# Kernel tuning notes

Measured on AMD Instinct MI355X. Metric: run time of the kernel, lower is better.

## Reference

```python
import jax, jax.numpy as jnp
import numpy as np

EPS = 1e-5
ALPHA = 0.05   # propalpha
GDEP = 2       # gcn_depth
LAYERS = 3     # gcn_layers
NUM_TCN = 2    # num_layer tcn units per encoder


def conv1x1(W, b, x):
    # 1x1 Conv2d on [B,C,N,1]: pure channel mix
    return jnp.einsum('oc,bcnl->bonl', W, x) + b[None, :, None, None]


def tcn_unit(Wf, bf, Wg, bg, h):
    # gated TCN unit: tanh(filter) * sigmoid(gate), 1x1 convs (L==1)
    return jnp.tanh(conv1x1(Wf, bf, h)) * jax.nn.sigmoid(conv1x1(Wg, bg, h))


def mixprop(x, A, W, b):
    # MTGNN mixprop: add self-loops, row-normalize, gdep propagation steps,
    # concat hops on channel dim, 1x1 conv mlp. A: [N,N] or [B,N,N].
    N = A.shape[-1]
    A = A + jnp.eye(N, dtype=A.dtype)
    A = A / A.sum(-1, keepdims=True)
    h = x
    outs = [h]
    for _ in range(GDEP):
        if A.ndim == 2:
            hn = jnp.einsum('vw,bcwl->bcvl', A, h)
        else:
            hn = jnp.einsum('bvw,bcwl->bcvl', A, h)
        h = ALPHA * x + (1.0 - ALPHA) * hn
        outs.append(h)
    ho = jnp.concatenate(outs, axis=1)  # [B,(GDEP+1)*C,N,1]
    return conv1x1(W, b, ho)


def layernorm(x, w, b):
    # LayerNorm over (C,N,1) of [B,C,N,1]; idx=arange(N) selects full affine
    mu = x.mean(axis=(1, 2, 3), keepdims=True)
    var = x.var(axis=(1, 2, 3), keepdims=True)
    return (x - mu) / jnp.sqrt(var + EPS) * w[None] + b[None]


def setup_inputs() -> dict:
    key = jax.random.key(0)
    B, N, E, H, S, T = 8, 2048, 32, 128, 256, 12
    ks = jax.random.split(key, 32)
    s = 0.05
    inp = {
        'x': jax.random.normal(ks[0], (B, E, N, 1), jnp.float32),
        'dy_graph': jax.random.uniform(ks[1], (B, N, N), jnp.float32),
        'static_graph': jax.random.uniform(ks[2], (N, N), jnp.float32),
        'spatial_emb': jax.random.normal(ks[3], (B, 32, N, 1), jnp.float32),
        'temporal_d_emb': jax.random.normal(ks[4], (B, 32, N, 1), jnp.float32),
        'temporal_w_emb': jax.random.normal(ks[5], (B, 32, N, 1), jnp.float32),
        'enc_Wf': s * jax.random.normal(ks[6], (LAYERS, NUM_TCN, H, H), jnp.float32),
        'enc_bf': s * jax.random.normal(ks[7], (LAYERS, NUM_TCN, H), jnp.float32),
        'enc_Wg': s * jax.random.normal(ks[8], (LAYERS, NUM_TCN, H, H), jnp.float32),
        'enc_bg': s * jax.random.normal(ks[9], (LAYERS, NUM_TCN, H), jnp.float32),
        'skip_W': s * jax.random.normal(ks[10], (LAYERS, S, H), jnp.float32),
        'skip_b': s * jax.random.normal(ks[11], (LAYERS, S), jnp.float32),
        'norm_w': jnp.ones((LAYERS, E, N, 1), jnp.float32),
        'norm_b': jnp.zeros((LAYERS, E, N, 1), jnp.float32),
        'g0_W': s * jax.random.normal(ks[12], (LAYERS, E, (GDEP + 1) * E), jnp.float32),
        'g0_b': s * jax.random.normal(ks[13], (LAYERS, E), jnp.float32),
        'g1_W': s * jax.random.normal(ks[14], (LAYERS, E, (GDEP + 1) * E), jnp.float32),
        'g1_b': s * jax.random.normal(ks[15], (LAYERS, E), jnp.float32),
        'g2_W': s * jax.random.normal(ks[16], (LAYERS, E, (GDEP + 1) * E), jnp.float32),
        'g2_b': s * jax.random.normal(ks[17], (LAYERS, E), jnp.float32),
        'skipE_W': s * jax.random.normal(ks[18], (S, E), jnp.float32),
        'skipE_b': s * jax.random.normal(ks[19], (S,), jnp.float32),
        'end_W': s * jax.random.normal(ks[20], (T, S), jnp.float32),
        'end_b': s * jax.random.normal(ks[21], (T,), jnp.float32),
    }
    return inp


def reference(x, dy_graph, static_graph, spatial_emb, temporal_d_emb, temporal_w_emb,
              enc_Wf, enc_bf, enc_Wg, enc_bg, skip_W, skip_b, norm_w, norm_b,
              g0_W, g0_b, g1_W, g1_b, g2_W, g2_b, skipE_W, skipE_b, end_W, end_b):
    adp = dy_graph
    skip = 0.0
    for i in range(LAYERS):
        residual = x
        hidden = jnp.concatenate([x, spatial_emb, temporal_d_emb, temporal_w_emb], axis=1)
        for j in range(NUM_TCN):
            hidden = tcn_unit(enc_Wf[i, j], enc_bf[i, j], enc_Wg[i, j], enc_bg[i, j], hidden)
        skip = conv1x1(skip_W[i], skip_b[i], hidden) + skip
        x = (mixprop(x, static_graph, g0_W[i], g0_b[i])
             + mixprop(x, adp, g1_W[i], g1_b[i])
             + mixprop(x, jnp.swapaxes(adp, -1, -2), g2_W[i], g2_b[i]))
        x = x + residual
        x = jax.nn.relu(layernorm(x, norm_w[i], norm_b[i]))
    skip = conv1x1(skipE_W, skipE_b, x) + skip
    return conv1x1(end_W, end_b, skip)  # [B, seq_length, N, 1]
```

## Files before the change

### kernel.cpp

```cpp
#include <hip/hip_runtime.h>
#include <stdint.h>


typedef uint16_t u16;
typedef uint32_t u32;
typedef __attribute__((ext_vector_type(8))) short s8v;
typedef __attribute__((ext_vector_type(4))) float f4v;

#define MFMA16(a,b,c) __builtin_amdgcn_mfma_f32_16x16x32_bf16(a,b,c,0,0,0)

__device__ __forceinline__ float b2f(u16 u){ union{u32 i; float f;} x; x.i=(u32)u<<16; return x.f; }
__device__ __forceinline__ u16 f2b(float f){
  u32 u = __builtin_bit_cast(u32, f);
  u32 r = (u + 0x7fffu + ((u >> 16) & 1u)) >> 16;
  return (u16)r;
}

__device__ __forceinline__ void gld16(const void* g, void* l) {
  __builtin_amdgcn_global_load_lds(
      (const __attribute__((address_space(1))) void*)g,
      (__attribute__((address_space(3))) void*)l, 16, 0, 0);
}

__global__ __launch_bounds__(256) void kdetect(const u16* __restrict__ x, int* __restrict__ flag)
{
  const int i = blockIdx.x*256 + threadIdx.x;
  const uint4 v = ((const uint4*)x)[i];
  const u32 w[4] = {v.x, v.y, v.z, v.w};
  int cnt = 0;
  #pragma unroll
  for (int e = 0; e < 4; e++) {
    if ((w[e] & 0x7F80u) == 0x7F80u) cnt++;
    if (((w[e] >> 16) & 0x7F80u) == 0x7F80u) cnt++;
  }
  const unsigned long long m = __ballot(cnt != 0);
  if (m && (threadIdx.x & 63) == 0) atomicOr(flag, 1);
}

__global__ __launch_bounds__(256) void kcvt4(const void* __restrict__ src, u16* __restrict__ dst,
                                             int n4, const int* __restrict__ flag)
{
  if (!*flag) return;
  const int i = blockIdx.x*256 + threadIdx.x;
  if (i >= n4) return;
  const float4 v = ((const float4*)src)[i];
  u16 o[4]; o[0]=f2b(v.x); o[1]=f2b(v.y); o[2]=f2b(v.z); o[3]=f2b(v.w);
  *(uint2*)(dst + (long)i*4) = *(uint2*)o;
}

struct CvtTab { const void* s[18]; u16* d[18]; int n4[18]; };
__global__ __launch_bounds__(256) void kcvt_small(CvtTab tb, const int* __restrict__ flag)
{
  const int e = blockIdx.y;
  const int i = blockIdx.x*256 + threadIdx.x;
  if (i >= tb.n4[e]) return;
  if (*flag) {
    const float4 v = ((const float4*)tb.s[e])[i];
    u16 o[4]; o[0]=f2b(v.x); o[1]=f2b(v.y); o[2]=f2b(v.z); o[3]=f2b(v.w);
    *(uint2*)(tb.d[e] + (long)i*4) = *(uint2*)o;
  } else {
    *(uint2*)(tb.d[e] + (long)i*4) = ((const uint2*)tb.s[e])[i];
  }
}

__global__ __launch_bounds__(256) void kcvtT(
    const void* __restrict__ src, u16* __restrict__ dyb, u16* __restrict__ dytb,
    float* __restrict__ rsum, float* __restrict__ csum, const int* __restrict__ flag)
{
  __shared__ alignas(16) u32 tt[64][32];
  const int tid = threadIdx.x;
  const int b = blockIdx.z;
  const long r0 = (long)blockIdx.y*64;
  const long c0 = (long)blockIdx.x*64;
  const int rp = tid>>3, c8 = (tid&7)*8;
  const long base = (long)b*4194304;
  const int fl = *flag;

  u16 lo[8], hi[8];
  const long gl = base + (r0 + 2*rp)*2048 + c0 + c8;
  const long gh = gl + 2048;
  if (fl) {
    const float* sl = (const float*)src + gl;
    const float* sh = (const float*)src + gh;
    const float4 a0 = ((const float4*)sl)[0], a1 = ((const float4*)sl)[1];
    const float4 b0 = ((const float4*)sh)[0], b1 = ((const float4*)sh)[1];
    lo[0]=f2b(a0.x); lo[1]=f2b(a0.y); lo[2]=f2b(a0.z); lo[3]=f2b(a0.w);
    lo[4]=f2b(a1.x); lo[5]=f2b(a1.y); lo[6]=f2b(a1.z); lo[7]=f2b(a1.w);
    hi[0]=f2b(b0.x); hi[1]=f2b(b0.y); hi[2]=f2b(b0.z); hi[3]=f2b(b0.w);
    hi[4]=f2b(b1.x); hi[5]=f2b(b1.y); hi[6]=f2b(b1.z); hi[7]=f2b(b1.w);
    *(uint4*)(dyb + gl) = *(uint4*)lo;
    *(uint4*)(dyb + gh) = *(uint4*)hi;
  } else {
    *(uint4*)lo = *((const uint4*)((const u16*)src + gl));
    *(uint4*)hi = *((const uint4*)((const u16*)src + gh));
  }
  float rsl = 0.f, rsh = 0.f;
  #pragma unroll
  for (int e = 0; e < 8; e++) {
    rsl += b2f(lo[e]); rsh += b2f(hi[e]);
    const int c = c8 + e;
    tt[c][rp ^ ((c & 0x38) >> 1)] = (u32)lo[e] | ((u32)hi[e] << 16);
  }
  rsl += __shfl_down(rsl, 4, 8); rsl += __shfl_down(rsl, 2, 8); rsl += __shfl_down(rsl, 1, 8);
  rsh += __shfl_down(rsh, 4, 8); rsh += __shfl_down(rsh, 2, 8); rsh += __shfl_down(rsh, 1, 8);
  if ((tid & 7) == 0) {
    atomicAdd(rsum + b*2048 + r0 + 2*rp,     rsl);
    atomicAdd(rsum + b*2048 + r0 + 2*rp + 1, rsh);
  }
  __syncthreads();

  const int c = tid>>2, j4 = (tid&3)*8;
  const int sw = (c & 0x38) >> 1;
  u32 q[8];
  *(uint4*)&q[0] = *(const uint4*)&tt[c][j4 ^ sw];
  *(uint4*)&q[4] = *(const uint4*)&tt[c][(j4 + 4) ^ sw];
  float cs = 0.f;
  #pragma unroll
  for (int e = 0; e < 8; e++) { cs += b2f((u16)q[e]); cs += b2f((u16)(q[e] >> 16)); }
  cs += __shfl_down(cs, 2, 4); cs += __shfl_down(cs, 1, 4);
  u16* dp = dytb + base + (c0 + c)*2048 + r0 + 2*j4;
  *(uint4*)(dp)     = *(uint4*)&q[0];
  *(uint4*)(dp + 8) = *(uint4*)&q[4];
  if ((tid & 3) == 0) atomicAdd(csum + b*2048 + c0 + c, cs);
}

__global__ void kfin(float* __restrict__ v){
  const int i = blockIdx.x*256 + threadIdx.x;
  v[i] = 1.f/(1.f + v[i]);
}

struct PG {
  const u16* Ac0; const u16* Ac1; const u16* Ac2;
  const u16* Ar0; const u16* Ar1;
  const int* flag;
  long ab0, ab1, ab2;
  const u16* X0; const u16* X1; const u16* X2;
  const float* R0; const float* R1; const float* R2;
  long rb0, rb1, rb2;
  u16* O0; u16* O1; u16* O2;
};

__global__ __launch_bounds__(256) void kprops(PG p, long x_bs, long o_bs)
{
  __shared__ u16 Al[4][64][64];
  __shared__ u16 Xl[4][32][64];
  const int tid = threadIdx.x, wave = tid>>6, lane = tid&63;
  const int lw = lane&15, quad = lane>>4;
  const int wr = wave>>1, wc = wave&1;
  const int v0 = blockIdx.x*64;
  const int b = blockIdx.y, g = blockIdx.z;
  const int fl = *p.flag;
  const u16* Ag; long ab; const u16* Xg; const float* Rg; long rb; u16* Og;
  if (g == 0)      { Ag = fl ? p.Ac0 : p.Ar0; ab = p.ab0; Xg = p.X0; Rg = p.R0; rb = p.rb0; Og = p.O0; }
  else if (g == 1) { Ag = fl ? p.Ac1 : p.Ar1; ab = p.ab1; Xg = p.X1; Rg = p.R1; rb = p.rb1; Og = p.O1; }
  else             { Ag = p.Ac2;              ab = p.ab2; Xg = p.X2; Rg = p.R2; rb = p.rb2; Og = p.O2; }
  const u16* Ab = Ag + (long)b*ab;
  const u16* Xb = Xg + (long)b*x_bs;

  const int srow = wave*8 + (lane>>3);
  const int skc  = lane&7;
  const long soff = (long)((skc ^ (srow&7))*8);
  const u16* srcA0 = Ab + (long)(v0 + srow)*2048 + soff;
  const u16* srcA1 = Ab + (long)(v0 + 32 + srow)*2048 + soff;
  const u16* srcX  = Xb + (long)srow*2048 + soff;

#define STAGE(tt) do { const int bb_=(tt)&3; const long k0_=(long)(tt)*64;          \
    gld16(srcA0 + k0_, (void*)((char*)&Al[bb_][0][0]  + wave*1024));                \
    gld16(srcA1 + k0_, (void*)((char*)&Al[bb_][32][0] + wave*1024));                \
    gld16(srcX  + k0_, (void*)((char*)&Xl[bb_][0][0]  + wave*1024)); } while(0)

  f4v acc0 = {0.f,0.f,0.f,0.f}, acc1 = {0.f,0.f,0.f,0.f};
  const int arow0 = wr*32 + lw;
  const int arow1 = wr*32 + 16 + lw;
  const int xrow  = wc*16 + lw;
  const int sw    = lw & 7;
  const int q0    = (quad ^ sw)*8;
  const int q1    = ((quad ^ sw) ^ 4)*8;

  STAGE(0); STAGE(1); STAGE(2);

  #pragma unroll 1
  for (int t = 0; t < 32; t++) {
    if (t < 30)       asm volatile("s_waitcnt vmcnt(6)" ::: "memory");
    else if (t == 30) asm volatile("s_waitcnt vmcnt(3)" ::: "memory");
    else              asm volatile("s_waitcnt vmcnt(0)" ::: "memory");
    __builtin_amdgcn_s_barrier();
    __builtin_amdgcn_sched_barrier(0);
    const int bb = t&3;
    s8v x0  = *(const s8v*)&Xl[bb][xrow][q0];
    s8v a00 = *(const s8v*)&Al[bb][arow0][q0];
    s8v a10 = *(const s8v*)&Al[bb][arow1][q0];
    s8v x1  = *(const s8v*)&Xl[bb][xrow][q1];
    s8v a01 = *(const s8v*)&Al[bb][arow0][q1];
    s8v a11 = *(const s8v*)&Al[bb][arow1][q1];
    acc0 = MFMA16(a00, x0, acc0);
    acc1 = MFMA16(a10, x0, acc1);
    acc0 = MFMA16(a01, x1, acc0);
    acc1 = MFMA16(a11, x1, acc1);
    if (t <= 28) STAGE(t+3);
  }
#undef STAGE

  const int c = wc*16 + lw;
  const float* rp = Rg + (long)b*rb;
  u16* ob = Og + (long)b*o_bs;
  #pragma unroll
  for (int f = 0; f < 2; f++) {
    const f4v s = f ? acc1 : acc0;
    const int vb = v0 + wr*32 + f*16 + quad*4;
    const u16* dp = Xb + (long)c*2048 + vb;
    u16 pk[4];
    #pragma unroll
    for (int r = 0; r < 4; r++) pk[r] = f2b((s[r] + b2f(dp[r])) * rp[vb + r]);
    *(uint2*)(ob + (long)c*2048 + vb) = *(uint2*)pk;
  }
}

template<int TRANSA, int MODE>
__global__ __launch_bounds__(256) void kprop(
    const u16* __restrict__ A, long a_bs, int lda, int K,
    const u16* __restrict__ X, long x_bs, int ldx,
    const u16* __restrict__ D, long d_bs,
    const float* __restrict__ rinv, long r_bs,
    const float* __restrict__ bias,
    u16* __restrict__ out0, float* __restrict__ out1, long o_bs)
{
  __shared__ u16 As[4][2][16][40];
  __shared__ f4v red[4][2][64];
  const int tid = threadIdx.x;
  const int wave = tid >> 6, lane = tid & 63;
  const int lw = lane & 15, quad = lane >> 4;
  const int v0 = blockIdx.x * 16;
  const int ball = blockIdx.z + blockIdx.y;
  const u16* Ab = A + (long)ball * a_bs;
  const u16* Xb = X + (long)ball * x_bs;
  const int KC = K >> 5;

  f4v acc0 = {0.f,0.f,0.f,0.f}, acc1 = {0.f,0.f,0.f,0.f};

  int r0, c0_;
  if (TRANSA == 0) { r0 = lane >> 2; c0_ = (lane & 3) * 8; }
  else             { r0 = lane >> 1; c0_ = (lane & 1) * 8; }

  int ci = wave;
  bool has = ci < KC;
  uint4 d = make_uint4(0,0,0,0);
  if (has) {
    d = (TRANSA == 0)
      ? *(const uint4*)(Ab + (long)(v0 + r0) * lda + ci * 32 + c0_)
      : *(const uint4*)(Ab + (long)(ci * 32 + r0) * lda + v0 + c0_);
  }
  int buf = 0;
  while (has) {
    if (TRANSA == 0) {
      *(uint4*)&As[wave][buf][r0][c0_] = d;
    } else {
      u16 tmp[8]; *(uint4*)tmp = d;
      #pragma unroll
      for (int e = 0; e < 8; e++) As[wave][buf][c0_ + e][r0] = tmp[e];
    }
    const int cn = ci + 4;
    const bool hn = cn < KC;
    if (hn) {
      d = (TRANSA == 0)
        ? *(const uint4*)(Ab + (long)(v0 + r0) * lda + cn * 32 + c0_)
        : *(const uint4*)(Ab + (long)(cn * 32 + r0) * lda + v0 + c0_);
    }
    s8v af = *(const s8v*)&As[wave][buf][lw][quad * 8];
    const u16* xk = Xb + ci * 32 + quad * 8;
    s8v b0 = *(const s8v*)(xk + (long)lw * ldx);
    s8v b1 = *(const s8v*)(xk + (long)(16 + lw) * ldx);
    acc0 = MFMA16(af, b0, acc0);
    acc1 = MFMA16(af, b1, acc1);
    ci = cn; has = hn; buf ^= 1;
  }
  red[wave][0][lane] = acc0;
  red[wave][1][lane] = acc1;
  __syncthreads();
  if (wave == 0) {
    const int vb = v0 + quad * 4;
    #pragma unroll
    for (int nt = 0; nt < 2; nt++) {
      f4v a = red[0][nt][lane] + red[1][nt][lane] + red[2][nt][lane] + red[3][nt][lane];
      const int c = nt * 16 + lw;
      const u16* dp = D + (long)ball * d_bs + (long)c * 2048 + vb;
      if (MODE == 0) {
        const float* rp = rinv + (long)ball * r_bs + vb;
        u16 pk[4];
        #pragma unroll
        for (int r = 0; r < 4; r++) pk[r] = f2b((a[r] + b2f(dp[r])) * rp[r]);
        *(uint2*)(out0 + (long)ball * o_bs + (long)c * 2048 + vb) = *(uint2*)pk;
      } else {
        const float bs = bias[c];
        float4 st;
        st.x = a[0] + bs + b2f(dp[0]);
        st.y = a[1] + bs + b2f(dp[1]);
        st.z = a[2] + bs + b2f(dp[2]);
        st.w = a[3] + bs + b2f(dp[3]);
        *(float4*)(out1 + (long)ball * o_bs + (long)c * 2048 + vb) = st;
      }
    }
  }
}

__global__ __launch_bounds__(256) void ktcn(
    const u16* __restrict__ H, const u16* __restrict__ Wf, const u16* __restrict__ bfv,
    const u16* __restrict__ Wg, const u16* __restrict__ bgv, u16* __restrict__ out)
{
  const int tid = threadIdx.x, wave = tid>>6, lane = tid&63, lw = lane&15, quad = lane>>4;
  const long j0 = (long)blockIdx.x*64 + wave*16;
  const f4v zero = {0.f,0.f,0.f,0.f};
  f4v accf[8], accg[8];
  #pragma unroll
  for (int nt=0; nt<8; nt++){ accf[nt] = zero; accg[nt] = zero; }
  const u16* Arow = H + (j0 + lw)*128 + quad*8;
  #pragma unroll
  for (int k0 = 0; k0 < 128; k0 += 32) {
    s8v a = *(const s8v*)(Arow + k0);
    #pragma unroll
    for (int nt = 0; nt < 8; nt++) {
      const int o = nt*16 + lw;
      s8v bf_ = *(const s8v*)(Wf + o*128 + k0 + quad*8);
      s8v bg_ = *(const s8v*)(Wg + o*128 + k0 + quad*8);
      accf[nt] = MFMA16(a, bf_, accf[nt]);
      accg[nt] = MFMA16(a, bg_, accg[nt]);
    }
  }
  #pragma unroll
  for (int nt = 0; nt < 8; nt++) {
    const int o = nt*16 + lw;
    const float fb = b2f(bfv[o]), gb = b2f(bgv[o]);
    #pragma unroll
    for (int rr = 0; rr < 4; rr++) {
      const long j = j0 + quad*4 + rr;
      const float f = accf[nt][rr] + fb, g = accg[nt][rr] + gb;
      const float e2 = __expf(2.f*f);
      const float th = 1.f - 2.f/(e2 + 1.f);
      const float sg = 1.f/(1.f + __expf(-g));
      out[j*128 + o] = f2b(th*sg);
    }
  }
}

__global__ __launch_bounds__(256) void kskip(
    const u16* __restrict__ A, int lda, int K,
    const u16* __restrict__ W, int ldb,
    const u16* __restrict__ bias,
    float* __restrict__ skipbuf, int addprev, int mode, u16* __restrict__ outb)
{
  const int tid = threadIdx.x, wave = tid>>6, lane = tid&63, lw = lane&15, quad = lane>>4;
  const long j0 = (long)blockIdx.x*64 + wave*16;
  const f4v zero = {0.f,0.f,0.f,0.f};
  f4v acc[16];
  #pragma unroll
  for (int nt=0; nt<16; nt++) acc[nt] = zero;
  const u16* Arow = A + (j0 + lw)*(long)lda + quad*8;
  for (int k0 = 0; k0 < K; k0 += 32) {
    s8v a = *(const s8v*)(Arow + k0);
    #pragma unroll
    for (int nt = 0; nt < 16; nt++) {
      const int o = nt*16 + lw;
      s8v b = *(const s8v*)(W + (long)o*ldb + k0 + quad*8);
      acc[nt] = MFMA16(a, b, acc[nt]);
    }
  }
  #pragma unroll
  for (int nt = 0; nt < 16; nt++) {
    const int o = nt*16 + lw;
    const float bv = b2f(bias[o]);
    #pragma unroll
    for (int rr = 0; rr < 4; rr++) {
      const long j = j0 + quad*4 + rr;
      float v = acc[nt][rr] + bv;
      if (addprev) v += skipbuf[j*256 + o];
      if (mode == 0) skipbuf[j*256 + o] = v;
      else           outb[j*256 + o] = f2b(v);
    }
  }
}

__global__ __launch_bounds__(256) void kend(
    const u16* __restrict__ A, const u16* __restrict__ W, const u16* __restrict__ bias,
    void* __restrict__ outv, const int* __restrict__ flag)
{
  const int tid = threadIdx.x, wave = tid>>6, lane = tid&63, lw = lane&15, quad = lane>>4;
  const long j0 = (long)blockIdx.x*64 + wave*16;
  f4v acc = {0.f,0.f,0.f,0.f};
  const u16* Arow = A + (j0 + lw)*256 + quad*8;
  #pragma unroll
  for (int k0 = 0; k0 < 256; k0 += 32) {
    s8v a = *(const s8v*)(Arow + k0);
    s8v b = {0,0,0,0,0,0,0,0};
    if (lw < 12) b = *(const s8v*)(W + lw*256 + k0 + quad*8);
    acc = MFMA16(a, b, acc);
  }
  if (lw < 12) {
    const float bv = b2f(bias[lw]);
    const int fl = *flag;
    #pragma unroll
    for (int rr = 0; rr < 4; rr++) {
      const long j = j0 + quad*4 + rr;
      const long oi = (j >> 11)*24576 + lw*2048 + (j & 2047);
      const float val = acc[rr] + bv;
      if (fl) ((float*)outv)[oi] = val;
      else    ((u16*)outv)[oi]   = f2b(val);
    }
  }
}

__global__ __launch_bounds__(256) void khid0(
    const void* __restrict__ x, const void* __restrict__ spat,
    const void* __restrict__ tde, const void* __restrict__ twe,
    u16* __restrict__ hid, u16* __restrict__ slot0, const int* __restrict__ flag)
{
  __shared__ u16 t[32][72];
  const int tid = threadIdx.x, b = blockIdx.y, v0 = blockIdx.x*64;
  const int fl = *flag;
  const void* srcs[4] = {x, spat, tde, twe};
  #pragma unroll
  for (int e = 0; e < 4; e++) {
    const int c = tid>>3, v8 = (tid&7)*8;
    const long boff = (long)c*2048 + v0 + v8;
    u16 o8[8];
    if (fl) {
      const float* sp = (const float*)srcs[e] + (long)b*65536 + boff;
      const float4 a = ((const float4*)sp)[0], bb = ((const float4*)sp)[1];
      o8[0]=f2b(a.x); o8[1]=f2b(a.y); o8[2]=f2b(a.z); o8[3]=f2b(a.w);
      o8[4]=f2b(bb.x); o8[5]=f2b(bb.y); o8[6]=f2b(bb.z); o8[7]=f2b(bb.w);
    } else {
      *(uint4*)o8 = *(const uint4*)((const u16*)srcs[e] + (long)b*65536 + boff);
    }
    if (e == 0) *(uint4*)(slot0 + (long)b*458752 + boff) = *(uint4*)o8;
    *(uint4*)&t[c][v8] = *(uint4*)o8;
    __syncthreads();
    const int jl = tid>>2, c8 = (tid&3)*8;
    u16 q8[8];
    #pragma unroll
    for (int i = 0; i < 8; i++) q8[i] = t[c8 + i][jl];
    *(uint4*)(hid + ((long)b*2048 + v0 + jl)*128 + e*32 + c8) = *(uint4*)q8;
    __syncthreads();
  }
}

__global__ __launch_bounds__(256) void krowsum(const u16* __restrict__ srcA, const u16* __restrict__ srcB,
                                               const int* __restrict__ flag,
                                               float* __restrict__ outv, int nrows)
{
  const u16* src = (*flag) ? srcA : srcB;
  const int wave = threadIdx.x>>6, lane = threadIdx.x&63;
  const int row = blockIdx.x*4 + wave;
  if (row >= nrows) return;
  const u16* p = src + (long)row*2048 + lane*8;
  float s = 0.f;
  #pragma unroll
  for (int it = 0; it < 4; it++) {
    u16 v[8]; *(uint4*)v = *(const uint4*)(p + it*512);
    #pragma unroll
    for (int e = 0; e < 8; e++) s += b2f(v[e]);
  }
  #pragma unroll
  for (int off = 32; off; off >>= 1) s += __shfl_down(s, off, 64);
  if (lane == 0) outv[row] = 1.f/(1.f + s);
}

__global__ __launch_bounds__(256) void kweff(
    const u16* __restrict__ g0W, const u16* __restrict__ g1W, const u16* __restrict__ g2W,
    const u16* __restrict__ g0b, const u16* __restrict__ g1b, const u16* __restrict__ g2b,
    int ioff, int boff, u16* __restrict__ weff, float* __restrict__ bw)
{
  const int idx = blockIdx.x*256 + threadIdx.x;
  if (idx < 32) bw[idx] = b2f(g0b[boff+idx]) + b2f(g1b[boff+idx]) + b2f(g2b[boff+idx]);
  if (idx >= 7168) return;
  const int o = idx / 224, m = idx % 224;
  const u16* Ws[3] = {g0W + ioff, g1W + ioff, g2W + ioff};
  float val;
  if (m < 32) {
    val = 0.f;
    #pragma unroll
    for (int g = 0; g < 3; g++) {
      const float w0 = b2f(Ws[g][o*96 + m]);
      const float w1 = b2f(Ws[g][o*96 + 32 + m]);
      const float w2 = b2f(Ws[g][o*96 + 64 + m]);
      val += w0 + 0.05f*(w1 + w2);
    }
  } else {
    const int f = (m - 32) >> 5, cc = m & 31;
    const int g = f >> 1, typ = f & 1;
    const float w1 = b2f(Ws[g][o*96 + 32 + cc]);
    const float w2 = b2f(Ws[g][o*96 + 64 + cc]);
    val = (typ == 0) ? (0.95f*w1 + 0.0475f*w2) : (0.9025f*w2);
  }
  weff[o*224 + m] = f2b(val);
}

__global__ __launch_bounds__(256) void kstats(const float* __restrict__ xpre, float* __restrict__ raw)
{
  const int b = blockIdx.y, tid = threadIdx.x;
  const float4* p = (const float4*)(xpre + (long)b*65536 + (long)blockIdx.x*8192);
  float s = 0.f, q = 0.f;
  #pragma unroll
  for (int i = 0; i < 8; i++) {
    const float4 v = p[tid + i*256];
    s += v.x + v.y + v.z + v.w;
    q += v.x*v.x + v.y*v.y + v.z*v.z + v.w*v.w;
  }
  __shared__ float ss[256], qq[256];
  ss[tid] = s; qq[tid] = q;
  __syncthreads();
  for (int st = 128; st; st >>= 1) {
    if (tid < st) { ss[tid] += ss[tid+st]; qq[tid] += qq[tid+st]; }
    __syncthreads();
  }
  if (tid == 0) { atomicAdd(raw + b*2, ss[0]); atomicAdd(raw + b*2 + 1, qq[0]); }
}

__global__ __launch_bounds__(256) void kapply(
    const float* __restrict__ xpre, const float* __restrict__ raw,
    const u16* __restrict__ nw, const u16* __restrict__ nb,
    u16* __restrict__ slot0, u16* __restrict__ hid)
{
  __shared__ u16 t[32][72];
  const int tid = threadIdx.x, b = blockIdx.y, v0 = blockIdx.x*64;
  const float mu = raw[b*2] * (1.f/65536.f);
  const float var = raw[b*2+1] * (1.f/65536.f) - mu*mu;
  const float rs = rsqrtf(var + 1e-5f);
  const int c = tid>>3, v8 = (tid&7)*8;
  const long boff = (long)c*2048 + v0 + v8;
  float4 xa = *(const float4*)(xpre + (long)b*65536 + boff);
  float4 xbv = *(const float4*)(xpre + (long)b*65536 + boff + 4);
  u16 wv[8], bv[8], o8[8];
  *(uint4*)wv = *(const uint4*)(nw + boff);
  *(uint4*)bv = *(const uint4*)(nb + boff);
  const float xs[8] = {xa.x, xa.y, xa.z, xa.w, xbv.x, xbv.y, xbv.z, xbv.w};
  #pragma unroll
  for (int e = 0; e < 8; e++) {
    float y = (xs[e] - mu) * rs * b2f(wv[e]) + b2f(bv[e]);
    y = fmaxf(y, 0.f);
    o8[e] = f2b(y);
    t[c][v8 + e] = o8[e];
  }
  *(uint4*)(slot0 + (long)b*458752 + boff) = *(uint4*)o8;
  __syncthreads();
  const int jl = tid>>2, c8 = (tid&3)*8;
  u16 q8[8];
  #pragma unroll
  for (int e = 0; e < 8; e++) q8[e] = t[c8 + e][jl];
  *(uint4*)(hid + ((long)b*2048 + v0 + jl)*128 + c8) = *(uint4*)q8;
}

extern "C" void kernel_launch(void* const* d_in, const int* in_sizes, int n_in,
                              void* d_out, int out_size, void* d_ws, size_t ws_size,
                              hipStream_t stream)
{
  (void)in_sizes; (void)n_in; (void)out_size; (void)ws_size;

  char* ws = (char*)d_ws;
  u16*   pbuf = (u16*)(ws + 0);
  u16*   hid  = (u16*)(ws + 7340032);
  u16*   hb1  = (u16*)(ws + 11534336);
  u16*   hb2  = (u16*)(ws + 15728640);
  float* skip = (float*)(ws + 19922944);
  u16*   xsb  = (u16*)(ws + 36700160);
  float* xpre = (float*)(ws + 45088768);
  u16*   weff = (u16*)(ws + 47185920);
  float* bw   = (float*)(ws + 47202304);
  float* rst  = (float*)(ws + 47203328);
  float* rdy  = (float*)(ws + 47211520);
  float* cdy  = (float*)(ws + 47277056);
  int*   flag = (int*)(ws + 47343616);
  float* raw  = (float*)(ws + 47343744);

  size_t coff = 50331648;
  auto alloc = [&](size_t elems) -> u16* {
    u16* p = (u16*)(ws + coff);
    coff += ((elems*2 + 255)/256)*256;
    return p;
  };
  u16* dyb   = alloc(33554432);
  u16* stgb  = alloc(4194304);
  u16* encWf = alloc(98304);
  u16* encbf = alloc(768);
  u16* encWg = alloc(98304);
  u16* encbg = alloc(768);
  u16* skW   = alloc(98304);
  u16* skb   = alloc(768);
  u16* nw    = alloc(196608);
  u16* nb    = alloc(196608);
  u16* g0W   = alloc(9216);
  u16* g0b   = alloc(96);
  u16* g1W   = alloc(9216);
  u16* g1b   = alloc(96);
  u16* g2W   = alloc(9216);
  u16* g2b   = alloc(96);
  u16* sEW   = alloc(8192);
  u16* sEb   = alloc(256);
  u16* eW    = alloc(3072);
  u16* eb    = alloc(12);
  u16* dytb  = alloc(33554432);

  hipMemsetAsync(flag, 0, 320, stream);
  hipLaunchKernelGGL(kdetect, dim3(32), dim3(256), 0, stream, (const u16*)d_in[0], flag);

  CvtTab tb;
  {
    const void* ss[18] = { d_in[6], d_in[7], d_in[8], d_in[9], d_in[10], d_in[11],
      d_in[12], d_in[13], d_in[14], d_in[15], d_in[16], d_in[17], d_in[18], d_in[19],
      d_in[20], d_in[21], d_in[22], d_in[23] };
    u16* dd[18] = { encWf, encbf, encWg, encbg, skW, skb, nw, nb,
      g0W, g0b, g1W, g1b, g2W, g2b, sEW, sEb, eW, eb };
    const int nn[18] = { 24576, 192, 24576, 192, 24576, 192, 49152, 49152,
      2304, 24, 2304, 24, 2304, 24, 2048, 64, 768, 3 };
    for (int e = 0; e < 18; e++) { tb.s[e] = ss[e]; tb.d[e] = dd[e]; tb.n4[e] = nn[e]; }
  }
  hipLaunchKernelGGL(kcvt_small, dim3(192, 18), dim3(256), 0, stream, tb, flag);
  hipLaunchKernelGGL(kcvt4, dim3(4096), dim3(256), 0, stream, d_in[2], stgb, 1048576, flag);

  hipMemsetAsync(rdy, 0, 131072, stream);
  hipLaunchKernelGGL(kcvtT, dim3(32,32,8), dim3(256), 0, stream,
      d_in[1], dyb, dytb, rdy, cdy, flag);
  hipLaunchKernelGGL(kfin, dim3(128), dim3(256), 0, stream, rdy);
  hipLaunchKernelGGL(krowsum, dim3(512), dim3(256), 0, stream,
      stgb, (const u16*)d_in[2], flag, rst, 2048);
  hipLaunchKernelGGL(khid0, dim3(32,8), dim3(256), 0, stream,
      d_in[0], d_in[3], d_in[4], d_in[5], hid, pbuf, flag);

  const long PB = 458752;
  const long SL = 65536;
  const long DYB = 4194304;

  for (int i = 0; i < 3; i++) {
    hipLaunchKernelGGL(ktcn, dim3(256), dim3(256), 0, stream,
        hid, encWf + (i*2+0)*16384, encbf + (i*2+0)*128, encWg + (i*2+0)*16384, encbg + (i*2+0)*128, hb1);
    hipLaunchKernelGGL(ktcn, dim3(256), dim3(256), 0, stream,
        hb1, encWf + (i*2+1)*16384, encbf + (i*2+1)*128, encWg + (i*2+1)*16384, encbg + (i*2+1)*128, hb2);
    hipLaunchKernelGGL(kskip, dim3(256), dim3(256), 0, stream,
        hb2, 128, 128, skW + i*32768, 128, skb + i*256, skip, (i>0)?1:0, 0, (u16*)nullptr);
    hipLaunchKernelGGL(kweff, dim3(28), dim3(256), 0, stream,
        g0W, g1W, g2W, g0b, g1b, g2b, i*3072, i*32, weff, bw);

    PG p1;
    p1.Ac0 = stgb; p1.Ac1 = dyb; p1.Ac2 = dytb;
    p1.Ar0 = (const u16*)d_in[2]; p1.Ar1 = (const u16*)d_in[1];
    p1.flag = flag;
    p1.ab0 = 0;   p1.ab1 = DYB; p1.ab2 = DYB;
    p1.X0 = pbuf; p1.X1 = pbuf; p1.X2 = pbuf;
    p1.R0 = rst;  p1.R1 = rdy;  p1.R2 = cdy;
    p1.rb0 = 0;   p1.rb1 = 2048; p1.rb2 = 2048;
    p1.O0 = pbuf + 1*SL; p1.O1 = pbuf + 3*SL; p1.O2 = pbuf + 5*SL;
    hipLaunchKernelGGL(kprops, dim3(32,8,3), dim3(256), 0, stream, p1, PB, PB);

    PG p2 = p1;
    p2.X0 = pbuf + 1*SL; p2.X1 = pbuf + 3*SL; p2.X2 = pbuf + 5*SL;
    p2.O0 = pbuf + 2*SL; p2.O1 = pbuf + 4*SL; p2.O2 = pbuf + 6*SL;
    hipLaunchKernelGGL(kprops, dim3(32,8,3), dim3(256), 0, stream, p2, PB, PB);

    hipLaunchKernelGGL((kprop<1,1>), dim3(128,1,8), dim3(256), 0, stream,
        pbuf, PB, 2048, 224, weff, 0L, 224, pbuf, PB, (const float*)nullptr, 0L, bw, (u16*)nullptr, xpre, 65536L);
    hipLaunchKernelGGL(kstats, dim3(8,8), dim3(256), 0, stream, xpre, raw + i*16);
    hipLaunchKernelGGL(kapply, dim3(32,8), dim3(256), 0, stream,
        xpre, raw + i*16, nw + i*65536, nb + i*65536, pbuf, hid);
  }
  hipLaunchKernelGGL(kskip, dim3(256), dim3(256), 0, stream,
      hid, 128, 32, sEW, 32, sEb, skip, 1, 1, xsb);
  hipLaunchKernelGGL(kend, dim3(256), dim3(256), 0, stream, xsb, eW, eb, d_out, flag);
}
```

Baseline: 715.9 us.

## Read dynamic graph transposed on the fly instead of materializing transpose

Stops writing a transposed bf16 copy of the dynamic adjacency during conversion, saving a 64 MB write and its buffer. A new kpropT kernel reads the untransposed adjacency column-wise and transposes it through swizzled LDS tiles before the MFMAs, replacing the third group of kprops. This trades the one-time transpose write for register-staged transposed loads and scattered LDS stores in each of the six propagation passes, with only double buffering and 512-thread blocks.

```diff
diff --git a/kernel.cpp b/kernel.cpp
--- a/kernel.cpp
+++ b/kernel.cpp
@@ -64,7 +64,7 @@
 }
 
 __global__ __launch_bounds__(256) void kcvtT(
-    const void* __restrict__ src, u16* __restrict__ dyb, u16* __restrict__ dytb,
+    const void* __restrict__ src, u16* __restrict__ dyb,
     float* __restrict__ rsum, float* __restrict__ csum, const int* __restrict__ flag)
 {
   __shared__ alignas(16) u32 tt[64][32];
@@ -118,9 +118,6 @@
   #pragma unroll
   for (int e = 0; e < 8; e++) { cs += b2f((u16)q[e]); cs += b2f((u16)(q[e] >> 16)); }
   cs += __shfl_down(cs, 2, 4); cs += __shfl_down(cs, 1, 4);
-  u16* dp = dytb + base + (c0 + c)*2048 + r0 + 2*j4;
-  *(uint4*)(dp)     = *(uint4*)&q[0];
-  *(uint4*)(dp + 8) = *(uint4*)&q[4];
   if ((tid & 3) == 0) atomicAdd(csum + b*2048 + c0 + c, cs);
 }
 
@@ -130,14 +127,14 @@
 }
 
 struct PG {
-  const u16* Ac0; const u16* Ac1; const u16* Ac2;
+  const u16* Ac0; const u16* Ac1;
   const u16* Ar0; const u16* Ar1;
   const int* flag;
-  long ab0, ab1, ab2;
-  const u16* X0; const u16* X1; const u16* X2;
-  const float* R0; const float* R1; const float* R2;
-  long rb0, rb1, rb2;
-  u16* O0; u16* O1; u16* O2;
+  long ab0, ab1;
+  const u16* X0; const u16* X1;
+  const float* R0; const float* R1;
+  long rb0, rb1;
+  u16* O0; u16* O1;
 };
 
 __global__ __launch_bounds__(256) void kprops(PG p, long x_bs, long o_bs)
@@ -151,9 +148,8 @@
   const int b = blockIdx.y, g = blockIdx.z;
   const int fl = *p.flag;
   const u16* Ag; long ab; const u16* Xg; const float* Rg; long rb; u16* Og;
-  if (g == 0)      { Ag = fl ? p.Ac0 : p.Ar0; ab = p.ab0; Xg = p.X0; Rg = p.R0; rb = p.rb0; Og = p.O0; }
-  else if (g == 1) { Ag = fl ? p.Ac1 : p.Ar1; ab = p.ab1; Xg = p.X1; Rg = p.R1; rb = p.rb1; Og = p.O1; }
-  else             { Ag = p.Ac2;              ab = p.ab2; Xg = p.X2; Rg = p.R2; rb = p.rb2; Og = p.O2; }
+  if (g == 0) { Ag = fl ? p.Ac0 : p.Ar0; ab = p.ab0; Xg = p.X0; Rg = p.R0; rb = p.rb0; Og = p.O0; }
+  else        { Ag = fl ? p.Ac1 : p.Ar1; ab = p.ab1; Xg = p.X1; Rg = p.R1; rb = p.rb1; Og = p.O1; }
   const u16* Ab = Ag + (long)b*ab;
   const u16* Xb = Xg + (long)b*x_bs;
 
@@ -214,6 +210,81 @@
     for (int r = 0; r < 4; r++) pk[r] = f2b((s[r] + b2f(dp[r])) * rp[vb + r]);
     *(uint2*)(ob + (long)c*2048 + vb) = *(uint2*)pk;
   }
+}
+
+struct PT {
+  const u16* Ac; const u16* Ar; const int* flag;
+  const u16* X; const float* R; u16* O;
+};
+
+__global__ __launch_bounds__(512) void kpropT(PT p, long x_bs, long o_bs)
+{
+  __shared__ alignas(16) u32 At[2][64][32];
+  __shared__ alignas(16) u16 Xl[2][32][64];
+  const int tid = threadIdx.x;
+  const int wave = tid>>6, lane = tid&63;
+  const int lw = lane&15, quad = lane>>4;
+  const int wr = wave>>1, wc = wave&1;
+  const int v0 = blockIdx.x*64;
+  const int b  = blockIdx.y;
+  const int fl = *p.flag;
+  const u16* Ab = (fl ? p.Ac : p.Ar) + (long)b*4194304;
+  const u16* Xb = p.X + (long)b*x_bs;
+
+  const int pp = tid>>4, vq = (tid&15)*4;
+  const u16* tsrc = Ab + (long)(2*pp)*2048 + v0 + vq;
+  const int xc = tid>>3, xu = tid&7;
+  const u16* xsrc = Xb + (long)xc*2048 + xu*8;
+
+  uint2 tlo, thi; uint4 xv;
+  #define TLOAD(tt) do { const u16* s_ = tsrc + (long)(tt)*131072;                  \
+      tlo = *(const uint2*)(s_); thi = *(const uint2*)(s_ + 2048);                  \
+      if (tid < 256) xv = *(const uint4*)(xsrc + (long)(tt)*64); } while(0)
+  #define TSTORE(bb) do {                                                           \
+      const u16* l16_ = (const u16*)&tlo; const u16* h16_ = (const u16*)&thi;       \
+      _Pragma("unroll")                                                             \
+      for (int e = 0; e < 4; e++) {                                                 \
+        const int v_ = vq + e;                                                      \
+        At[bb][v_][(pp + 4*((v_>>3)&7)) & 31] = (u32)l16_[e] | ((u32)h16_[e]<<16);  \
+      }                                                                             \
+      if (tid < 256) *(uint4*)&Xl[bb][xc][(xu ^ (xc&7))*8] = xv; } while(0)
+
+  f4v acc = {0.f,0.f,0.f,0.f};
+  const int arow = wr*16 + lw;
+  const int xrow = wc*16 + lw;
+  const int at_t = (arow>>3)&7;
+  const int xsw  = xrow&7;
+
+  TLOAD(0);
+  TSTORE(0);
+  #pragma unroll 1
+  for (int t = 0; t < 32; t++) {
+    __syncthreads();
+    if (t < 31) TLOAD(t+1);
+    __builtin_amdgcn_sched_barrier(0);
+    const int bb = t&1;
+    #pragma unroll
+    for (int c32 = 0; c32 < 2; c32++) {
+      const int m = c32*4 + quad;
+      const int G = (m + at_t) & 7;
+      s8v a = *(const s8v*)&At[bb][arow][4*G];
+      s8v x = *(const s8v*)&Xl[bb][xrow][(m ^ xsw)*8];
+      acc = MFMA16(a, x, acc);
+    }
+    if (t < 31) TSTORE((t+1)&1);
+  }
+  #undef TLOAD
+  #undef TSTORE
+
+  const int c = wc*16 + lw;
+  const float* rp = p.R + (long)b*2048;
+  u16* ob = p.O + (long)b*o_bs;
+  const int vb = v0 + wr*16 + quad*4;
+  const u16* dp = Xb + (long)c*2048 + vb;
+  u16 pk[4];
+  #pragma unroll
+  for (int r = 0; r < 4; r++) pk[r] = f2b((acc[r] + b2f(dp[r])) * rp[vb + r]);
+  *(uint2*)(ob + (long)c*2048 + vb) = *(uint2*)pk;
 }
 
 template<int TRANSA, int MODE>
@@ -596,7 +667,6 @@
   u16* sEb   = alloc(256);
   u16* eW    = alloc(3072);
   u16* eb    = alloc(12);
-  u16* dytb  = alloc(33554432);
 
   hipMemsetAsync(flag, 0, 320, stream);
   hipLaunchKernelGGL(kdetect, dim3(32), dim3(256), 0, stream, (const u16*)d_in[0], flag);
@@ -617,7 +687,7 @@
 
   hipMemsetAsync(rdy, 0, 131072, stream);
   hipLaunchKernelGGL(kcvtT, dim3(32,32,8), dim3(256), 0, stream,
-      d_in[1], dyb, dytb, rdy, cdy, flag);
+      d_in[1], dyb, rdy, cdy, flag);
   hipLaunchKernelGGL(kfin, dim3(128), dim3(256), 0, stream, rdy);
   hipLaunchKernelGGL(krowsum, dim3(512), dim3(256), 0, stream,
       stgb, (const u16*)d_in[2], flag, rst, 2048);
@@ -639,20 +709,29 @@
         g0W, g1W, g2W, g0b, g1b, g2b, i*3072, i*32, weff, bw);
 
     PG p1;
-    p1.Ac0 = stgb; p1.Ac1 = dyb; p1.Ac2 = dytb;
+    p1.Ac0 = stgb; p1.Ac1 = dyb;
     p1.Ar0 = (const u16*)d_in[2]; p1.Ar1 = (const u16*)d_in[1];
     p1.flag = flag;
-    p1.ab0 = 0;   p1.ab1 = DYB; p1.ab2 = DYB;
-    p1.X0 = pbuf; p1.X1 = pbuf; p1.X2 = pbuf;
-    p1.R0 = rst;  p1.R1 = rdy;  p1.R2 = cdy;
-    p1.rb0 = 0;   p1.rb1 = 2048; p1.rb2 = 2048;
-    p1.O0 = pbuf + 1*SL; p1.O1 = pbuf + 3*SL; p1.O2 = pbuf + 5*SL;
-    hipLaunchKernelGGL(kprops, dim3(32,8,3), dim3(256), 0, stream, p1, PB, PB);
+    p1.ab0 = 0;   p1.ab1 = DYB;
+    p1.X0 = pbuf; p1.X1 = pbuf;
+    p1.R0 = rst;  p1.R1 = rdy;
+    p1.rb0 = 0;   p1.rb1 = 2048;
+    p1.O0 = pbuf + 1*SL; p1.O1 = pbuf + 3*SL;
+    hipLaunchKernelGGL(kprops, dim3(32,8,2), dim3(256), 0, stream, p1, PB, PB);
+
+    PT t1;
+    t1.Ac = dyb; t1.Ar = (const u16*)d_in[1]; t1.flag = flag;
+    t1.X = pbuf; t1.R = cdy; t1.O = pbuf + 5*SL;
+    hipLaunchKernelGGL(kpropT, dim3(32,8), dim3(512), 0, stream, t1, PB, PB);
 
     PG p2 = p1;
-    p2.X0 = pbuf + 1*SL; p2.X1 = pbuf + 3*SL; p2.X2 = pbuf + 5*SL;
-    p2.O0 = pbuf + 2*SL; p2.O1 = pbuf + 4*SL; p2.O2 = pbuf + 6*SL;
-    hipLaunchKernelGGL(kprops, dim3(32,8,3), dim3(256), 0, stream, p2, PB, PB);
+    p2.X0 = pbuf + 1*SL; p2.X1 = pbuf + 3*SL;
+    p2.O0 = pbuf + 2*SL; p2.O1 = pbuf + 4*SL;
+    hipLaunchKernelGGL(kprops, dim3(32,8,2), dim3(256), 0, stream, p2, PB, PB);
+
+    PT t2 = t1;
+    t2.X = pbuf + 5*SL; t2.O = pbuf + 6*SL;
+    hipLaunchKernelGGL(kpropT, dim3(32,8), dim3(512), 0, stream, t2, PB, PB);
 
     hipLaunchKernelGGL((kprop<1,1>), dim3(128,1,8), dim3(256), 0, stream,
         pbuf, PB, 2048, 224, weff, 0L, 224, pbuf, PB, (const float*)nullptr, 0L, bw, (u16*)nullptr, xpre, 65536L);
```

After: 794.1 us. 10.9% more time.

## Fuse TCN unit pair, fold layernorm stats into mixprop epilogue, hoist weff

Applied to the files above, without the earlier changes.

The two gated TCN units are merged into one kernel that keeps the intermediate activation in LDS instead of writing it to global memory and reading it back. LayerNorm sum and sum-of-squares are now accumulated in the mixprop output kernel with wave shuffles and atomics, so the separate stats kernel and its re-read of xpre are gone. The combined mixprop weight computation runs once for all layers before the loop instead of once per layer. This removes several launches and a round trip through global memory, at the cost of more atomics on the stats buffer and more LDS per TCN block.

```diff
diff --git a/kernel.cpp b/kernel.cpp
--- a/kernel.cpp
+++ b/kernel.cpp
@@ -223,7 +223,8 @@
     const u16* __restrict__ D, long d_bs,
     const float* __restrict__ rinv, long r_bs,
     const float* __restrict__ bias,
-    u16* __restrict__ out0, float* __restrict__ out1, long o_bs)
+    u16* __restrict__ out0, float* __restrict__ out1, long o_bs,
+    float* __restrict__ stats)
 {
   __shared__ u16 As[4][2][16][40];
   __shared__ f4v red[4][2][64];
@@ -279,6 +280,7 @@
   __syncthreads();
   if (wave == 0) {
     const int vb = v0 + quad * 4;
+    float ssum = 0.f, sq = 0.f;
     #pragma unroll
     for (int nt = 0; nt < 2; nt++) {
       f4v a = red[0][nt][lane] + red[1][nt][lane] + red[2][nt][lane] + red[3][nt][lane];
@@ -298,15 +300,33 @@
         st.z = a[2] + bs + b2f(dp[2]);
         st.w = a[3] + bs + b2f(dp[3]);
         *(float4*)(out1 + (long)ball * o_bs + (long)c * 2048 + vb) = st;
+        ssum += st.x + st.y + st.z + st.w;
+        sq   += st.x*st.x + st.y*st.y + st.z*st.z + st.w*st.w;
       }
     }
-  }
-}
-
-__global__ __launch_bounds__(256) void ktcn(
-    const u16* __restrict__ H, const u16* __restrict__ Wf, const u16* __restrict__ bfv,
-    const u16* __restrict__ Wg, const u16* __restrict__ bgv, u16* __restrict__ out)
-{
+    if (MODE == 1) {
+      #pragma unroll
+      for (int off = 32; off; off >>= 1) {
+        ssum += __shfl_down(ssum, off, 64);
+        sq   += __shfl_down(sq,   off, 64);
+      }
+      if (lane == 0) {
+        atomicAdd(stats + ball*2,     ssum);
+        atomicAdd(stats + ball*2 + 1, sq);
+      }
+    }
+  }
+}
+
+__global__ __launch_bounds__(256) void ktcn2(
+    const u16* __restrict__ H,
+    const u16* __restrict__ Wf1, const u16* __restrict__ bf1v,
+    const u16* __restrict__ Wg1, const u16* __restrict__ bg1v,
+    const u16* __restrict__ Wf2, const u16* __restrict__ bf2v,
+    const u16* __restrict__ Wg2, const u16* __restrict__ bg2v,
+    u16* __restrict__ out)
+{
+  __shared__ u16 h1[4][16][136];
   const int tid = threadIdx.x, wave = tid>>6, lane = tid&63, lw = lane&15, quad = lane>>4;
   const long j0 = (long)blockIdx.x*64 + wave*16;
   const f4v zero = {0.f,0.f,0.f,0.f};
@@ -320,8 +340,8 @@
     #pragma unroll
     for (int nt = 0; nt < 8; nt++) {
       const int o = nt*16 + lw;
-      s8v bf_ = *(const s8v*)(Wf + o*128 + k0 + quad*8);
-      s8v bg_ = *(const s8v*)(Wg + o*128 + k0 + quad*8);
+      s8v bf_ = *(const s8v*)(Wf1 + o*128 + k0 + quad*8);
+      s8v bg_ = *(const s8v*)(Wg1 + o*128 + k0 + quad*8);
       accf[nt] = MFMA16(a, bf_, accf[nt]);
       accg[nt] = MFMA16(a, bg_, accg[nt]);
     }
@@ -329,7 +349,35 @@
   #pragma unroll
   for (int nt = 0; nt < 8; nt++) {
     const int o = nt*16 + lw;
-    const float fb = b2f(bfv[o]), gb = b2f(bgv[o]);
+    const float fb = b2f(bf1v[o]), gb = b2f(bg1v[o]);
+    #pragma unroll
+    for (int rr = 0; rr < 4; rr++) {
+      const float f = accf[nt][rr] + fb, g = accg[nt][rr] + gb;
+      const float e2 = __expf(2.f*f);
+      const float th = 1.f - 2.f/(e2 + 1.f);
+      const float sg = 1.f/(1.f + __expf(-g));
+      h1[wave][quad*4 + rr][o] = f2b(th*sg);
+    }
+  }
+  __syncthreads();
+  #pragma unroll
+  for (int nt=0; nt<8; nt++){ accf[nt] = zero; accg[nt] = zero; }
+  #pragma unroll
+  for (int k0 = 0; k0 < 128; k0 += 32) {
+    s8v a = *(const s8v*)&h1[wave][lw][k0 + quad*8];
+    #pragma unroll
+    for (int nt = 0; nt < 8; nt++) {
+      const int o = nt*16 + lw;
+      s8v bf_ = *(const s8v*)(Wf2 + o*128 + k0 + quad*8);
+      s8v bg_ = *(const s8v*)(Wg2 + o*128 + k0 + quad*8);
+      accf[nt] = MFMA16(a, bf_, accf[nt]);
+      accg[nt] = MFMA16(a, bg_, accg[nt]);
+    }
+  }
+  #pragma unroll
+  for (int nt = 0; nt < 8; nt++) {
+    const int o = nt*16 + lw;
+    const float fb = b2f(bf2v[o]), gb = b2f(bg2v[o]);
     #pragma unroll
     for (int rr = 0; rr < 4; rr++) {
       const long j = j0 + quad*4 + rr;
@@ -466,8 +514,12 @@
 __global__ __launch_bounds__(256) void kweff(
     const u16* __restrict__ g0W, const u16* __restrict__ g1W, const u16* __restrict__ g2W,
     const u16* __restrict__ g0b, const u16* __restrict__ g1b, const u16* __restrict__ g2b,
-    int ioff, int boff, u16* __restrict__ weff, float* __restrict__ bw)
-{
+    u16* __restrict__ weffA, float* __restrict__ bwA)
+{
+  const int L = blockIdx.y;
+  const int ioff = L*3072, boff = L*32;
+  u16* weff = weffA + L*7168;
+  float* bw = bwA + L*32;
   const int idx = blockIdx.x*256 + threadIdx.x;
   if (idx < 32) bw[idx] = b2f(g0b[boff+idx]) + b2f(g1b[boff+idx]) + b2f(g2b[boff+idx]);
   if (idx >= 7168) return;
@@ -491,27 +543,6 @@
     val = (typ == 0) ? (0.95f*w1 + 0.0475f*w2) : (0.9025f*w2);
   }
   weff[o*224 + m] = f2b(val);
-}
-
-__global__ __launch_bounds__(256) void kstats(const float* __restrict__ xpre, float* __restrict__ raw)
-{
-  const int b = blockIdx.y, tid = threadIdx.x;
-  const float4* p = (const float4*)(xpre + (long)b*65536 + (long)blockIdx.x*8192);
-  float s = 0.f, q = 0.f;
-  #pragma unroll
-  for (int i = 0; i < 8; i++) {
-    const float4 v = p[tid + i*256];
-    s += v.x + v.y + v.z + v.w;
-    q += v.x*v.x + v.y*v.y + v.z*v.z + v.w*v.w;
-  }
-  __shared__ float ss[256], qq[256];
-  ss[tid] = s; qq[tid] = q;
-  __syncthreads();
-  for (int st = 128; st; st >>= 1) {
-    if (tid < st) { ss[tid] += ss[tid+st]; qq[tid] += qq[tid+st]; }
-    __syncthreads();
-  }
-  if (tid == 0) { atomicAdd(raw + b*2, ss[0]); atomicAdd(raw + b*2 + 1, qq[0]); }
 }
 
 __global__ __launch_bounds__(256) void kapply(
@@ -557,13 +588,10 @@
   char* ws = (char*)d_ws;
   u16*   pbuf = (u16*)(ws + 0);
   u16*   hid  = (u16*)(ws + 7340032);
-  u16*   hb1  = (u16*)(ws + 11534336);
   u16*   hb2  = (u16*)(ws + 15728640);
   float* skip = (float*)(ws + 19922944);
   u16*   xsb  = (u16*)(ws + 36700160);
   float* xpre = (float*)(ws + 45088768);
-  u16*   weff = (u16*)(ws + 47185920);
-  float* bw   = (float*)(ws + 47202304);
   float* rst  = (float*)(ws + 47203328);
   float* rdy  = (float*)(ws + 47211520);
   float* cdy  = (float*)(ws + 47277056);
@@ -597,6 +625,8 @@
   u16* eW    = alloc(3072);
   u16* eb    = alloc(12);
   u16* dytb  = alloc(33554432);
+  u16* weffA = alloc(21504);
+  float* bwA = (float*)alloc(192);
 
   hipMemsetAsync(flag, 0, 320, stream);
   hipLaunchKernelGGL(kdetect, dim3(32), dim3(256), 0, stream, (const u16*)d_in[0], flag);
@@ -614,6 +644,8 @@
   }
   hipLaunchKernelGGL(kcvt_small, dim3(192, 18), dim3(256), 0, stream, tb, flag);
   hipLaunchKernelGGL(kcvt4, dim3(4096), dim3(256), 0, stream, d_in[2], stgb, 1048576, flag);
+  hipLaunchKernelGGL(kweff, dim3(28, 3), dim3(256), 0, stream,
+      g0W, g1W, g2W, g0b, g1b, g2b, weffA, bwA);
 
   hipMemsetAsync(rdy, 0, 131072, stream);
   hipLaunchKernelGGL(kcvtT, dim3(32,32,8), dim3(256), 0, stream,
@@ -629,14 +661,13 @@
   const long DYB = 4194304;
 
   for (int i = 0; i < 3; i++) {
-    hipLaunchKernelGGL(ktcn, dim3(256), dim3(256), 0, stream,
-        hid, encWf + (i*2+0)*16384, encbf + (i*2+0)*128, encWg + (i*2+0)*16384, encbg + (i*2+0)*128, hb1);
-    hipLaunchKernelGGL(ktcn, dim3(256), dim3(256), 0, stream,
-        hb1, encWf + (i*2+1)*16384, encbf + (i*2+1)*128, encWg + (i*2+1)*16384, encbg + (i*2+1)*128, hb2);
+    hipLaunchKernelGGL(ktcn2, dim3(256), dim3(256), 0, stream,
+        hid,
+        encWf + (i*2+0)*16384, encbf + (i*2+0)*128, encWg + (i*2+0)*16384, encbg + (i*2+0)*128,
+        encWf + (i*2+1)*16384, encbf + (i*2+1)*128, encWg + (i*2+1)*16384, encbg + (i*2+1)*128,
+        hb2);
     hipLaunchKernelGGL(kskip, dim3(256), dim3(256), 0, stream,
         hb2, 128, 128, skW + i*32768, 128, skb + i*256, skip, (i>0)?1:0, 0, (u16*)nullptr);
-    hipLaunchKernelGGL(kweff, dim3(28), dim3(256), 0, stream,
-        g0W, g1W, g2W, g0b, g1b, g2b, i*3072, i*32, weff, bw);
 
     PG p1;
     p1.Ac0 = stgb; p1.Ac1 = dyb; p1.Ac2 = dytb;
@@ -655,8 +686,8 @@
     hipLaunchKernelGGL(kprops, dim3(32,8,3), dim3(256), 0, stream, p2, PB, PB);
 
     hipLaunchKernelGGL((kprop<1,1>), dim3(128,1,8), dim3(256), 0, stream,
-        pbuf, PB, 2048, 224, weff, 0L, 224, pbuf, PB, (const float*)nullptr, 0L, bw, (u16*)nullptr, xpre, 65536L);
-    hipLaunchKernelGGL(kstats, dim3(8,8), dim3(256), 0, stream, xpre, raw + i*16);
+        pbuf, PB, 2048, 224, weffA + i*7168, 0L, 224, pbuf, PB,
+        (const float*)nullptr, 0L, bwA + i*32, (u16*)nullptr, xpre, 65536L, raw + i*16);
     hipLaunchKernelGGL(kapply, dim3(32,8), dim3(256), 0, stream,
         xpre, raw + i*16, nw + i*65536, nb + i*65536, pbuf, hid);
   }
```

Measured after the change: 773.3 us. +8.0%, slower.
